# Optimization experiments

Measured on AMD Instinct MI355X. Metric: run time of the kernel, lower is better.

Reference implementation:

```python
import jax, jax.numpy as jnp
import numpy as np

FEATURE_DIM = 768
LAMBDA_REG = 0.01
NUM_ITERS = 5
LR = 0.1
SIGMA = 2.0
MARGIN = 1.0
BN_EPS = 1e-5


def setup_inputs() -> dict:
    key = jax.random.key(0)
    ks = jax.random.split(key, 10)
    B, D = 32, FEATURE_DIM
    search_features = jax.random.normal(ks[0], (B, D, 32, 32), dtype=jnp.float32)
    target_features = jax.random.normal(ks[1], (B, D, 16, 16), dtype=jnp.float32)
    target_mask = jax.random.uniform(ks[2], (B, 1, 16, 16), dtype=jnp.float32)
    conv_w = jax.random.normal(ks[3], (D, D), dtype=jnp.float32) * (1.0 / np.sqrt(D))
    conv_b = jax.random.normal(ks[4], (D,), dtype=jnp.float32) * 0.01
    bn_gamma = jnp.ones((D,), dtype=jnp.float32)
    bn_beta = jnp.zeros((D,), dtype=jnp.float32)
    bn_mean = jax.random.normal(ks[5], (D,), dtype=jnp.float32) * 0.01
    bn_var = jax.random.uniform(ks[6], (D,), dtype=jnp.float32, minval=0.5, maxval=1.5)
    filter_init = jax.random.normal(ks[7], (1, D, 1, 1), dtype=jnp.float32) * 0.01
    return {
        "search_features": search_features,
        "target_features": target_features,
        "target_mask": target_mask,
        "conv_w": conv_w,
        "conv_b": conv_b,
        "bn_gamma": bn_gamma,
        "bn_beta": bn_beta,
        "bn_mean": bn_mean,
        "bn_var": bn_var,
        "filter_init": filter_init,
    }


def _proj(x, conv_w, conv_b, bn_gamma, bn_beta, bn_mean, bn_var):
    # 1x1 conv == channel-wise GEMM, then BatchNorm (eval mode, running stats)
    y = jnp.einsum('bdhw,ed->behw', x, conv_w) + conv_b[None, :, None, None]
    inv_std = bn_gamma / jnp.sqrt(bn_var + BN_EPS)
    return (y - bn_mean[None, :, None, None]) * inv_std[None, :, None, None] + bn_beta[None, :, None, None]


def _gaussian_label(mask):
    B, _, H, W = mask.shape
    yy, xx = jnp.meshgrid(jnp.arange(H, dtype=jnp.float32), jnp.arange(W, dtype=jnp.float32), indexing='ij')
    yy = yy[None, None]  # (1,1,H,W)
    xx = xx[None, None]
    msum = jnp.clip(mask.sum(axis=(2, 3), keepdims=True), 1.0)
    cy = (mask * yy).sum(axis=(2, 3), keepdims=True) / msum
    cx = (mask * xx).sum(axis=(2, 3), keepdims=True) / msum
    return jnp.exp(-((xx - cx) ** 2 + (yy - cy) ** 2) / (2.0 * SIGMA ** 2))


def reference(search_features, target_features, target_mask, conv_w, conv_b,
              bn_gamma, bn_beta, bn_mean, bn_var, filter_init):
    sp = _proj(search_features, conv_w, conv_b, bn_gamma, bn_beta, bn_mean, bn_var)
    tp = _proj(target_features, conv_w, conv_b, bn_gamma, bn_beta, bn_mean, bn_var)
    B = tp.shape[0]
    label = _gaussian_label(target_mask)  # (B,1,H',W')
    f = jnp.broadcast_to(filter_init, (B,) + filter_init.shape[1:])  # (B,D,1,1)
    for _ in range(NUM_ITERS):
        response = (tp * f).sum(axis=1, keepdims=True)  # (B,1,H',W')
        loss = jnp.maximum(MARGIN - response * label, 0.0)
        grad = jnp.where(loss > 0, -label * target_mask, 0.0)
        grad = grad.mean(axis=(2, 3), keepdims=True)  # (B,1,1,1), broadcasts over D
        f = f - LR * (grad + LAMBDA_REG * f)
    return (sp * f).sum(axis=1, keepdims=True)  # (B,1,H,W)
```

## Files before the change

kernel.cpp:

```cpp
#include <hip/hip_runtime.h>
#include <math.h>

#define DD   768
#define BB   32
#define NTP  256
#define NSP  1024
#define NT   (BB*NTP)
#define NS   (BB*NSP)
#define ECH  48
#define CHE  (DD/ECH)

#define OFF_UP  0
#define OFF_VP  (OFF_UP + ECH*DD)
#define OFF_U   (OFF_VP + ECH*DD)
#define OFF_V   (OFF_U + DD)
#define OFF_K   (OFF_V + DD)
#define OFF_TR0 (OFF_K + 64)
#define OFF_TS0 (OFF_TR0 + NT)
#define OFF_SR  (OFF_TS0 + NT)
#define OFF_SS  (OFF_SR + NS)

#define A5 0.99500999000499900f

__global__ void k_prep(const float* __restrict__ w, const float* __restrict__ cb,
                       const float* __restrict__ gamma, const float* __restrict__ beta,
                       const float* __restrict__ mean, const float* __restrict__ var,
                       const float* __restrict__ fi, float* __restrict__ ws) {
    int bx = blockIdx.x;
    int t = threadIdx.x;
    if (bx < ECH) {
        __shared__ float wu[CHE], wv[CHE];
        if (t < CHE) {
            int e = bx * CHE + t;
            float inv = gamma[e] / sqrtf(var[e] + 1e-5f);
            wv[t] = inv;
            wu[t] = inv * fi[e];
        }
        __syncthreads();
        if (t < 192) {
            const float4* w4 = (const float4*)w;
            float4 Ru = {0,0,0,0}, Rv = {0,0,0,0};
            #pragma unroll
            for (int j = 0; j < CHE; ++j) {
                float4 x = w4[(size_t)(bx * CHE + j) * 192 + t];
                float a = wu[j], b = wv[j];
                Ru.x += x.x * a; Ru.y += x.y * a; Ru.z += x.z * a; Ru.w += x.w * a;
                Rv.x += x.x * b; Rv.y += x.y * b; Rv.z += x.z * b; Rv.w += x.w * b;
            }
            *(float4*)(ws + OFF_UP + bx * DD + t * 4) = Ru;
            *(float4*)(ws + OFF_VP + bx * DD + t * 4) = Rv;
        }
    } else {
        __shared__ float r1[256], r2[256];
        float a1 = 0.f, a2 = 0.f;
        for (int e = t; e < DD; e += 256) {
            float inv = gamma[e] / sqrtf(var[e] + 1e-5f);
            float x = (cb[e] - mean[e]) * inv + beta[e];
            a1 += x * fi[e];
            a2 += x;
        }
        r1[t] = a1; r2[t] = a2;
        __syncthreads();
        for (int s = 128; s > 0; s >>= 1) {
            if (t < s) { r1[t] += r1[t + s]; r2[t] += r2[t + s]; }
            __syncthreads();
        }
        if (t == 0) { ws[OFF_K] = r1[0]; ws[OFF_K + 1] = r2[0]; }
    }
}

__global__ void k_prep2(float* __restrict__ ws) {
    int bx = blockIdx.x;
    int d = (bx % 3) * 256 + threadIdx.x;
    int isV = bx / 3;
    int srcOff = isV ? OFF_VP : OFF_UP;
    int dstOff = isV ? OFF_V : OFF_U;
    float a = 0.f;
    #pragma unroll 8
    for (int ec = 0; ec < ECH; ++ec) a += ws[srcOff + ec * DD + d];
    ws[dstOff + d] = a;
}

__global__ __launch_bounds__(256) void k_big(const float* __restrict__ sf,
                                             const float* __restrict__ tf,
                                             float* __restrict__ ws) {
    int bx = blockIdx.x;
    int lb = (bx & 7) * 80 + (bx >> 3);
    int t = threadIdx.x;
    int px = t & 15, sub = t >> 4;
    __shared__ float su[DD], sv[DD];
    for (int i = t; i < DD; i += 256) { su[i] = ws[OFF_U + i]; sv[i] = ws[OFF_V + i]; }
    __syncthreads();

    const float4* base;
    int STR;
    float4 *oR, *oS;
    if (lb < 512) {
        int pf = lb * 16 + px;
        int b = pf >> 8;
        base = (const float4*)sf + ((size_t)b * DD + sub * 48) * (NSP/4) + (pf & 255);
        STR = NSP / 4;
        oR = (float4*)(ws + OFF_SR) + pf;
        oS = (float4*)(ws + OFF_SS) + pf;
    } else {
        int pf = (lb - 512) * 16 + px;
        int b = pf >> 6;
        base = (const float4*)tf + ((size_t)b * DD + sub * 48) * (NTP/4) + (pf & 63);
        STR = NTP / 4;
        oR = (float4*)(ws + OFF_TR0) + pf;
        oS = (float4*)(ws + OFF_TS0) + pf;
    }
    float4 accR = {0,0,0,0}, accS = {0,0,0,0};
    float4 buf[8];
    #pragma unroll
    for (int k = 0; k < 8; ++k) buf[k] = base[(size_t)k * STR];
    #pragma unroll
    for (int g = 1; g < 6; ++g) {
        float4 nxt[8];
        #pragma unroll
        for (int k = 0; k < 8; ++k) nxt[k] = base[(size_t)(g * 8 + k) * STR];
        #pragma unroll
        for (int k = 0; k < 8; ++k) {
            int ch = sub * 48 + (g - 1) * 8 + k;
            float u = su[ch], v = sv[ch];
            accR.x += buf[k].x * u; accR.y += buf[k].y * u; accR.z += buf[k].z * u; accR.w += buf[k].w * u;
            accS.x += buf[k].x * v; accS.y += buf[k].y * v; accS.z += buf[k].z * v; accS.w += buf[k].w * v;
            buf[k] = nxt[k];
        }
    }
    #pragma unroll
    for (int k = 0; k < 8; ++k) {
        int ch = sub * 48 + 40 + k;
        float u = su[ch], v = sv[ch];
        accR.x += buf[k].x * u; accR.y += buf[k].y * u; accR.z += buf[k].z * u; accR.w += buf[k].w * u;
        accS.x += buf[k].x * v; accS.y += buf[k].y * v; accS.z += buf[k].z * v; accS.w += buf[k].w * v;
    }
    __shared__ float4 redR[16][16], redS[16][16];
    redR[sub][px] = accR; redS[sub][px] = accS;
    __syncthreads();
    for (int s = 8; s > 0; s >>= 1) {
        if (sub < s) {
            float4 a = redR[sub + s][px], m = redR[sub][px];
            m.x += a.x; m.y += a.y; m.z += a.z; m.w += a.w; redR[sub][px] = m;
            float4 c = redS[sub + s][px], n = redS[sub][px];
            n.x += c.x; n.y += c.y; n.z += c.z; n.w += c.w; redS[sub][px] = n;
        }
        __syncthreads();
    }
    if (sub == 0) { *oR = redR[0][px]; *oS = redS[0][px]; }
}

__global__ void k_final(const float* __restrict__ mask, const float* __restrict__ ws,
                        float* __restrict__ out) {
    int b = blockIdx.x;
    int p = threadIdx.x;
    int lane = p & 63, wv = p >> 6;
    int h = p >> 4, w = p & 15;
    float K1 = ws[OFF_K], K2 = ws[OFF_K + 1];
    float r0 = K1 + ws[OFF_TR0 + b * 256 + p];
    float s0 = K2 + ws[OFF_TS0 + b * 256 + p];
    float m = mask[b * 256 + p];
    __shared__ float cross[4];
    auto bsum = [&](float v) -> float {
        #pragma unroll
        for (int o = 32; o > 0; o >>= 1) v += __shfl_xor(v, o, 64);
        if (lane == 0) cross[wv] = v;
        __syncthreads();
        float r = cross[0] + cross[1] + cross[2] + cross[3];
        __syncthreads();
        return r;
    };
    float msum = bsum(m);
    float sy = bsum(m * (float)h);
    float sx = bsum(m * (float)w);
    msum = fmaxf(msum, 1.0f);
    float cy = sy / msum, cx = sx / msum;
    float dx = (float)w - cx, dy = (float)h - cy;
    float label = expf(-(dx * dx + dy * dy) * 0.125f);
    float A = 1.0f, c = 0.0f;
    const float decay = 1.0f - 0.1f * 0.01f;
    #pragma unroll
    for (int it = 0; it < 5; ++it) {
        float resp = A * r0 + c * s0;
        float gc = (1.0f - resp * label > 0.0f) ? (-label * m) : 0.0f;
        float g = bsum(gc) * (1.0f / 256.0f);
        c = decay * c - 0.1f * g;
        A *= decay;
    }
    int g4 = b * 256 + p;
    float4 R = ((const float4*)(ws + OFF_SR))[g4];
    float4 S = ((const float4*)(ws + OFF_SS))[g4];
    float4 o;
    o.x = A5 * (K1 + R.x) + c * (K2 + S.x);
    o.y = A5 * (K1 + R.y) + c * (K2 + S.y);
    o.z = A5 * (K1 + R.z) + c * (K2 + S.z);
    o.w = A5 * (K1 + R.w) + c * (K2 + S.w);
    ((float4*)out)[g4] = o;
}

extern "C" void kernel_launch(void* const* d_in, const int* in_sizes, int n_in,
                              void* d_out, int out_size, void* d_ws, size_t ws_size,
                              hipStream_t stream) {
    const float* sf    = (const float*)d_in[0];
    const float* tf    = (const float*)d_in[1];
    const float* mask  = (const float*)d_in[2];
    const float* w     = (const float*)d_in[3];
    const float* cb    = (const float*)d_in[4];
    const float* gamma = (const float*)d_in[5];
    const float* beta  = (const float*)d_in[6];
    const float* mean  = (const float*)d_in[7];
    const float* var   = (const float*)d_in[8];
    const float* fi    = (const float*)d_in[9];
    float* out = (float*)d_out;
    float* ws  = (float*)d_ws;

    k_prep <<<ECH + 1, 256, 0, stream>>>(w, cb, gamma, beta, mean, var, fi, ws);
    k_prep2<<<6,       256, 0, stream>>>(ws);
    k_big  <<<640,     256, 0, stream>>>(sf, tf, ws);
    k_final<<<BB,      256, 0, stream>>>(mask, ws, out);
}
```

Measured before the change: 38.34 us.

## Fold prep2 reduction into main kernel and widen per-block pixel tiles

Removes the k_prep2 launch: each k_big block now sums the 16 partial U/V vectors itself when it loads them into shared memory. ECH drops from 48 to 16, so k_prep uses fewer, larger blocks. k_big is re-tiled so each block handles 128 pixels (32 float4 lanes) with 8 channel groups of 96 and 12-deep load buffers, halving the grid to 320 blocks and dropping the XCD block remap. This saves a launch and the per-block reduction overhead, but every block now redundantly re-reads the partials, and there are fewer blocks with more registers each.

```diff
diff --git a/kernel.cpp b/kernel.cpp
--- a/kernel.cpp
+++ b/kernel.cpp
@@ -7,14 +7,12 @@
 #define NSP  1024
 #define NT   (BB*NTP)
 #define NS   (BB*NSP)
-#define ECH  48
+#define ECH  16
 #define CHE  (DD/ECH)
 
 #define OFF_UP  0
 #define OFF_VP  (OFF_UP + ECH*DD)
-#define OFF_U   (OFF_VP + ECH*DD)
-#define OFF_V   (OFF_U + DD)
-#define OFF_K   (OFF_V + DD)
+#define OFF_K   (OFF_VP + ECH*DD)
 #define OFF_TR0 (OFF_K + 64)
 #define OFF_TS0 (OFF_TR0 + NT)
 #define OFF_SR  (OFF_TS0 + NT)
@@ -69,59 +67,59 @@
     }
 }
 
-__global__ void k_prep2(float* __restrict__ ws) {
-    int bx = blockIdx.x;
-    int d = (bx % 3) * 256 + threadIdx.x;
-    int isV = bx / 3;
-    int srcOff = isV ? OFF_VP : OFF_UP;
-    int dstOff = isV ? OFF_V : OFF_U;
-    float a = 0.f;
-    #pragma unroll 8
-    for (int ec = 0; ec < ECH; ++ec) a += ws[srcOff + ec * DD + d];
-    ws[dstOff + d] = a;
-}
-
 __global__ __launch_bounds__(256) void k_big(const float* __restrict__ sf,
                                              const float* __restrict__ tf,
                                              float* __restrict__ ws) {
     int bx = blockIdx.x;
-    int lb = (bx & 7) * 80 + (bx >> 3);
     int t = threadIdx.x;
-    int px = t & 15, sub = t >> 4;
+    int pxf4 = t & 31, sub = t >> 5;
     __shared__ float su[DD], sv[DD];
-    for (int i = t; i < DD; i += 256) { su[i] = ws[OFF_U + i]; sv[i] = ws[OFF_V + i]; }
+    if (t < 192) {
+        float4 U = {0,0,0,0}, V = {0,0,0,0};
+        #pragma unroll
+        for (int ec = 0; ec < ECH; ++ec) {
+            float4 a = ((const float4*)(ws + OFF_UP + ec * DD))[t];
+            float4 b = ((const float4*)(ws + OFF_VP + ec * DD))[t];
+            U.x += a.x; U.y += a.y; U.z += a.z; U.w += a.w;
+            V.x += b.x; V.y += b.y; V.z += b.z; V.w += b.w;
+        }
+        ((float4*)su)[t] = U;
+        ((float4*)sv)[t] = V;
+    }
     __syncthreads();
 
     const float4* base;
     int STR;
     float4 *oR, *oS;
-    if (lb < 512) {
-        int pf = lb * 16 + px;
-        int b = pf >> 8;
-        base = (const float4*)sf + ((size_t)b * DD + sub * 48) * (NSP/4) + (pf & 255);
+    if (bx < 256) {
+        int b = bx >> 3, q = bx & 7;
+        base = (const float4*)sf + ((size_t)b * DD + sub * 96) * (NSP/4) + q * 32 + pxf4;
         STR = NSP / 4;
-        oR = (float4*)(ws + OFF_SR) + pf;
-        oS = (float4*)(ws + OFF_SS) + pf;
+        int g4 = b * 256 + q * 32 + pxf4;
+        oR = (float4*)(ws + OFF_SR) + g4;
+        oS = (float4*)(ws + OFF_SS) + g4;
     } else {
-        int pf = (lb - 512) * 16 + px;
-        int b = pf >> 6;
-        base = (const float4*)tf + ((size_t)b * DD + sub * 48) * (NTP/4) + (pf & 63);
+        int u = bx - 256;
+        int b = u >> 1, q = u & 1;
+        base = (const float4*)tf + ((size_t)b * DD + sub * 96) * (NTP/4) + q * 32 + pxf4;
         STR = NTP / 4;
-        oR = (float4*)(ws + OFF_TR0) + pf;
-        oS = (float4*)(ws + OFF_TS0) + pf;
-    }
+        int g4 = b * 64 + q * 32 + pxf4;
+        oR = (float4*)(ws + OFF_TR0) + g4;
+        oS = (float4*)(ws + OFF_TS0) + g4;
+    }
+
     float4 accR = {0,0,0,0}, accS = {0,0,0,0};
-    float4 buf[8];
-    #pragma unroll
-    for (int k = 0; k < 8; ++k) buf[k] = base[(size_t)k * STR];
-    #pragma unroll
-    for (int g = 1; g < 6; ++g) {
-        float4 nxt[8];
-        #pragma unroll
-        for (int k = 0; k < 8; ++k) nxt[k] = base[(size_t)(g * 8 + k) * STR];
-        #pragma unroll
-        for (int k = 0; k < 8; ++k) {
-            int ch = sub * 48 + (g - 1) * 8 + k;
+    float4 buf[12];
+    #pragma unroll
+    for (int k = 0; k < 12; ++k) buf[k] = base[(size_t)k * STR];
+    #pragma unroll
+    for (int g = 1; g < 8; ++g) {
+        float4 nxt[12];
+        #pragma unroll
+        for (int k = 0; k < 12; ++k) nxt[k] = base[(size_t)(g * 12 + k) * STR];
+        #pragma unroll
+        for (int k = 0; k < 12; ++k) {
+            int ch = sub * 96 + (g - 1) * 12 + k;
             float u = su[ch], v = sv[ch];
             accR.x += buf[k].x * u; accR.y += buf[k].y * u; accR.z += buf[k].z * u; accR.w += buf[k].w * u;
             accS.x += buf[k].x * v; accS.y += buf[k].y * v; accS.z += buf[k].z * v; accS.w += buf[k].w * v;
@@ -129,25 +127,26 @@
         }
     }
     #pragma unroll
-    for (int k = 0; k < 8; ++k) {
-        int ch = sub * 48 + 40 + k;
+    for (int k = 0; k < 12; ++k) {
+        int ch = sub * 96 + 84 + k;
         float u = su[ch], v = sv[ch];
         accR.x += buf[k].x * u; accR.y += buf[k].y * u; accR.z += buf[k].z * u; accR.w += buf[k].w * u;
         accS.x += buf[k].x * v; accS.y += buf[k].y * v; accS.z += buf[k].z * v; accS.w += buf[k].w * v;
     }
-    __shared__ float4 redR[16][16], redS[16][16];
-    redR[sub][px] = accR; redS[sub][px] = accS;
+
+    __shared__ float4 redR[8][32], redS[8][32];
+    redR[sub][pxf4] = accR; redS[sub][pxf4] = accS;
     __syncthreads();
-    for (int s = 8; s > 0; s >>= 1) {
+    for (int s = 4; s > 0; s >>= 1) {
         if (sub < s) {
-            float4 a = redR[sub + s][px], m = redR[sub][px];
-            m.x += a.x; m.y += a.y; m.z += a.z; m.w += a.w; redR[sub][px] = m;
-            float4 c = redS[sub + s][px], n = redS[sub][px];
-            n.x += c.x; n.y += c.y; n.z += c.z; n.w += c.w; redS[sub][px] = n;
-        }
-        __syncthreads();
-    }
-    if (sub == 0) { *oR = redR[0][px]; *oS = redS[0][px]; }
+            float4 a = redR[sub + s][pxf4], m = redR[sub][pxf4];
+            m.x += a.x; m.y += a.y; m.z += a.z; m.w += a.w; redR[sub][pxf4] = m;
+            float4 c = redS[sub + s][pxf4], n = redS[sub][pxf4];
+            n.x += c.x; n.y += c.y; n.z += c.z; n.w += c.w; redS[sub][pxf4] = n;
+        }
+        __syncthreads();
+    }
+    if (sub == 0) { *oR = redR[0][pxf4]; *oS = redS[0][pxf4]; }
 }
 
 __global__ void k_final(const float* __restrict__ mask, const float* __restrict__ ws,
@@ -215,7 +214,6 @@
     float* ws  = (float*)d_ws;
 
     k_prep <<<ECH + 1, 256, 0, stream>>>(w, cb, gamma, beta, mean, var, fi, ws);
-    k_prep2<<<6,       256, 0, stream>>>(ws);
-    k_big  <<<640,     256, 0, stream>>>(sf, tf, ws);
+    k_big  <<<320,     256, 0, stream>>>(sf, tf, ws);
     k_final<<<BB,      256, 0, stream>>>(mask, ws, out);
 }
```

Result: faster. 35.92 us (-6.3%).
